# Kernel tuning notes

Measured on AMD Instinct MI355X. Metric: run time of the kernel, lower is better.

Reference implementation:

```python
import jax, jax.numpy as jnp
import numpy as np

D = 512
H = 8
HD = D // H
EPS = 1e-8


def setup_inputs() -> dict:
    key = jax.random.key(0)
    ks = jax.random.split(key, 16)
    B, S = 4, 2048
    s = lambda n: 1.0 / np.sqrt(n)
    inp = {
        "gene_emb": jax.random.normal(ks[0], (B, S, D), jnp.float32),
        "expr_emb": jax.random.normal(ks[1], (B, S, D), jnp.float32),
        "M": jax.random.uniform(ks[2], (B, S, S), jnp.float32),
        # weights stored (in, out) so y = x @ W + b
        "W_fused": jax.random.normal(ks[3], (2 * D, D), jnp.float32) * s(2 * D),
        "b_fused": jnp.zeros((D,), jnp.float32),
        "W_Q": jax.random.normal(ks[4], (D, D), jnp.float32) * s(D),
        "b_Q": jnp.zeros((D,), jnp.float32),
        "W_K": jax.random.normal(ks[5], (D, D), jnp.float32) * s(D),
        "b_K": jnp.zeros((D,), jnp.float32),
        "W_V": jax.random.normal(ks[6], (D, D), jnp.float32) * s(D),
        "b_V": jnp.zeros((D,), jnp.float32),
        "W_O": jax.random.normal(ks[7], (D, D), jnp.float32) * s(D),
        "b_O": jnp.zeros((D,), jnp.float32),
    }
    return inp


def reference(gene_emb, expr_emb, M, W_fused, b_fused, W_Q, b_Q, W_K, b_K, W_V, b_V, W_O, b_O):
    B, S, _ = gene_emb.shape
    scale = HD ** (-0.5)
    fused = jnp.concatenate([gene_emb, expr_emb], axis=-1) @ W_fused + b_fused
    # (B,S,D) -> (B,H,S,HD)
    split = lambda x: x.reshape(B, S, H, HD).transpose(0, 2, 1, 3)
    Q = split(fused @ W_Q + b_Q)
    K = split(fused @ W_K + b_K)
    V = split(expr_emb @ W_V + b_V)
    scores = jnp.einsum("bhqd,bhkd->bhqk", Q, K) * scale
    Mg = M[:, None, :, :]  # broadcast over heads
    scores = scores * Mg
    attn = jax.nn.softmax(scores, axis=-1)
    A_sparse = attn * Mg
    norm = jnp.sum(jnp.abs(A_sparse), axis=-1, keepdims=True) + EPS
    A_bar = A_sparse / norm
    out = jnp.einsum("bhqk,bhkd->bhqd", A_bar, V)
    out = out.transpose(0, 2, 1, 3).reshape(B, S, D)
    return out @ W_O + b_O
```

## Files before the change

kernel.cpp:

```cpp
#include <hip/hip_runtime.h>

typedef unsigned short u16;
typedef __attribute__((ext_vector_type(8))) short bf16x8_t;
typedef __attribute__((ext_vector_type(4))) float f32x4_t;
typedef __attribute__((ext_vector_type(16))) float f32x16_t;

__device__ __forceinline__ u16 f2bf(float x){
  union { float f; unsigned u; } v; v.f = x;
  unsigned r = v.u + 0x7FFFu + ((v.u >> 16) & 1u);
  return (u16)(r >> 16);
}
__device__ __forceinline__ float bf2f(u16 h){
  union { unsigned u; float f; } v; v.u = ((unsigned)h) << 16;
  return v.f;
}
__device__ __forceinline__ unsigned pack_hi16(float a, float b){
  union { float f; unsigned u; } x, y; x.f = a; y.f = b;
  return (x.u >> 16) | (y.u & 0xFFFF0000u);
}

__device__ __forceinline__ void gl2lds16(const u16* g, u16* l){
  __builtin_amdgcn_global_load_lds((const __attribute__((address_space(1))) void*)g,
                                   (__attribute__((address_space(3))) void*)l, 16, 0, 0);
}

__global__ __launch_bounds__(256) void split_concat_kernel(
    const float* __restrict__ gene, const float* __restrict__ expr,
    u16* __restrict__ Xh, u16* __restrict__ Xl)
{
  size_t e = ((size_t)blockIdx.x * 256 + threadIdx.x) * 4;
  int row = (int)(e >> 10);
  int col = (int)(e & 1023);
  const float* src = (col < 512) ? (gene + (size_t)row * 512 + col)
                                 : (expr + (size_t)row * 512 + (col - 512));
  float4 v = *(const float4*)src;
  float a[4] = {v.x, v.y, v.z, v.w};
  u16 hs[4], ls[4];
#pragma unroll
  for (int i = 0; i < 4; i++){
    hs[i] = f2bf(a[i]);
    ls[i] = f2bf(a[i] - bf2f(hs[i]));
  }
  *(uint2*)(Xh + e) = make_uint2(hs[0] | ((unsigned)hs[1] << 16), hs[2] | ((unsigned)hs[3] << 16));
  *(uint2*)(Xl + e) = make_uint2(ls[0] | ((unsigned)ls[1] << 16), ls[2] | ((unsigned)ls[3] << 16));
}

__global__ __launch_bounds__(256) void transpose_all_kernel(
    const float* __restrict__ Wf, const float* __restrict__ Wq,
    const float* __restrict__ Wk, const float* __restrict__ Wv,
    const float* __restrict__ Wo,
    u16* __restrict__ Wfth, u16* __restrict__ Wftl,
    u16* __restrict__ Wqth, u16* __restrict__ Wkth,
    u16* __restrict__ Wvth, u16* __restrict__ Woth)
{
  __shared__ float t[64][65];
  int id = blockIdx.x;
  const float* W; u16* Th; u16* Tl; int K, kx, ny;
  if (id < 128){ W = Wf; Th = Wfth; Tl = Wftl; K = 1024; kx = id >> 3; ny = id & 7; }
  else {
    int tt = id - 128; int wi = tt >> 6; tt &= 63; kx = tt >> 3; ny = tt & 7; K = 512;
    W  = (wi == 0) ? Wq  : (wi == 1) ? Wk  : (wi == 2) ? Wv  : Wo;
    Th = (wi == 0) ? Wqth: (wi == 1) ? Wkth: (wi == 2) ? Wvth: Woth;
    Tl = nullptr;
  }
  int k0 = kx * 64, n0 = ny * 64;
  int tid = threadIdx.x;
  int r = tid >> 4;
  int c4 = (tid & 15) * 4;
#pragma unroll
  for (int p = 0; p < 4; p++){
    int k = p * 16 + r;
    float4 v = *(const float4*)(W + (size_t)(k0 + k) * 512 + n0 + c4);
    t[c4 + 0][k] = v.x; t[c4 + 1][k] = v.y; t[c4 + 2][k] = v.z; t[c4 + 3][k] = v.w;
  }
  __syncthreads();
#pragma unroll
  for (int p = 0; p < 4; p++){
    int n = p * 16 + r;
    u16 hs[4], ls[4];
#pragma unroll
    for (int i = 0; i < 4; i++){
      float x = t[n][c4 + i];
      hs[i] = f2bf(x);
      ls[i] = f2bf(x - bf2f(hs[i]));
    }
    size_t o = (size_t)(n0 + n) * K + k0 + c4;
    *(uint2*)(Th + o) = make_uint2(hs[0] | ((unsigned)hs[1] << 16), hs[2] | ((unsigned)hs[3] << 16));
    if (Tl)
      *(uint2*)(Tl + o) = make_uint2(ls[0] | ((unsigned)ls[1] << 16), ls[2] | ((unsigned)ls[3] << 16));
  }
}

template<int SPLITS, int MODE, int DUAL>
__global__ __launch_bounds__(256, 2) void gemm_kernel(
    const u16* __restrict__ Ah, const u16* __restrict__ Al, int lda,
    const u16* __restrict__ Bh0, const u16* __restrict__ Bl0,
    const u16* __restrict__ Bh1, int K,
    const float* __restrict__ bias0, const float* __restrict__ bias1,
    void* __restrict__ out0, void* __restrict__ out1, void* __restrict__ outsec,
    float sc0, float sc1)
{
  __shared__ __align__(16) u16 sAh[128 * 32];
  __shared__ __align__(16) u16 sAl[SPLITS >= 2 ? 128 * 32 : 8];
  __shared__ __align__(16) u16 sBh[64 * 32];
  __shared__ __align__(16) u16 sBl[SPLITS == 3 ? 64 * 32 : 8];
  int tid = threadIdx.x;
  int lane = tid & 63, w = tid >> 6, quad = lane >> 4, l15 = lane & 15;
  int wm = w & 1, wn = w >> 1;
  int lid = (int)(blockIdx.y * gridDim.x + blockIdx.x);
  int side = DUAL ? (lid >> 9) : 0;
  int l = lid & 511;
  int m0 = (((l & 7) << 3) | ((l >> 3) & 7)) * 128;
  int n0 = (l >> 6) * 64;
  const u16* Bh = (DUAL && side) ? Bh1 : Bh0;
  const float* bias = (DUAL && side) ? bias1 : bias0;
  void* o0 = (DUAL && side) ? outsec : out0;
  float sc = (DUAL && side) ? sc1 : sc0;

  f32x4_t acc[4][2];
#pragma unroll
  for (int i = 0; i < 4; i++)
#pragma unroll
    for (int j = 0; j < 2; j++)
#pragma unroll
      for (int r = 0; r < 4; r++) acc[i][j][r] = 0.f;

  int lrow = lane >> 2;
  int swzS = ((lane >> 2) & 3) ^ ((lane >> 4) & 3);
  int gkq  = ((lane & 3) ^ swzS) * 8;
  const u16* pAh0 = Ah + (size_t)(m0 + w * 32 + lrow) * lda + gkq;
  const u16* pAh1 = Ah + (size_t)(m0 + w * 32 + 16 + lrow) * lda + gkq;
  const u16* pAl0 = (SPLITS >= 2) ? Al + (size_t)(m0 + w * 32 + lrow) * lda + gkq : nullptr;
  const u16* pAl1 = (SPLITS >= 2) ? Al + (size_t)(m0 + w * 32 + 16 + lrow) * lda + gkq : nullptr;
  const u16* pBh0 = Bh + (size_t)(n0 + w * 16 + lrow) * K + gkq;
  const u16* pBl0 = (SPLITS == 3) ? Bl0 + (size_t)(n0 + w * 16 + lrow) * K + gkq : nullptr;
  u16* dAh = sAh + w * 1024;
  u16* dAl = sAl + w * 1024;
  u16* dBh = sBh + w * 512;
  u16* dBl = sBl + w * 512;

  int pq = (quad ^ ((l15 & 3) ^ ((l15 >> 2) & 3))) * 8;

  for (int k0 = 0; k0 < K; k0 += 32){
    __syncthreads();
    gl2lds16(pAh0 + k0, dAh);
    gl2lds16(pAh1 + k0, dAh + 512);
    if constexpr (SPLITS >= 2){
      gl2lds16(pAl0 + k0, dAl);
      gl2lds16(pAl1 + k0, dAl + 512);
    }
    gl2lds16(pBh0 + k0, dBh);
    if constexpr (SPLITS == 3)
      gl2lds16(pBl0 + k0, dBl);
    __syncthreads();

    bf16x8_t aH[4], aL[4], bH[2], bL[2];
#pragma unroll
    for (int mi = 0; mi < 4; mi++){
      int ad = (wm * 64 + mi * 16 + l15) * 32 + pq;
      aH[mi] = *(const bf16x8_t*)&sAh[ad];
      if constexpr (SPLITS >= 2) aL[mi] = *(const bf16x8_t*)&sAl[ad];
    }
#pragma unroll
    for (int ni = 0; ni < 2; ni++){
      int bd = (wn * 32 + ni * 16 + l15) * 32 + pq;
      bH[ni] = *(const bf16x8_t*)&sBh[bd];
      if constexpr (SPLITS == 3) bL[ni] = *(const bf16x8_t*)&sBl[bd];
    }
#pragma unroll
    for (int mi = 0; mi < 4; mi++)
#pragma unroll
      for (int ni = 0; ni < 2; ni++){
        acc[mi][ni] = __builtin_amdgcn_mfma_f32_16x16x32_bf16(aH[mi], bH[ni], acc[mi][ni], 0, 0, 0);
        if constexpr (SPLITS == 3)
          acc[mi][ni] = __builtin_amdgcn_mfma_f32_16x16x32_bf16(aH[mi], bL[ni], acc[mi][ni], 0, 0, 0);
        if constexpr (SPLITS >= 2)
          acc[mi][ni] = __builtin_amdgcn_mfma_f32_16x16x32_bf16(aL[mi], bH[ni], acc[mi][ni], 0, 0, 0);
      }
  }

#pragma unroll
  for (int mi = 0; mi < 4; mi++)
#pragma unroll
    for (int ni = 0; ni < 2; ni++){
      int gn = n0 + wn * 32 + ni * 16 + l15;
      float bs = bias[gn];
      int gm0 = m0 + wm * 64 + mi * 16 + quad * 4;
#pragma unroll
      for (int r = 0; r < 4; r++){
        float v = acc[mi][ni][r] + bs;
        int gm = gm0 + r;
        if constexpr (MODE == 0){
          u16 hb = f2bf(v);
          ((u16*)o0)[(size_t)gm * 512 + gn] = hb;
          ((u16*)out1)[(size_t)gm * 512 + gn] = f2bf(v - bf2f(hb));
        } else if constexpr (MODE == 1){
          ((u16*)o0)[(size_t)gm * 512 + gn] = f2bf(v * sc);
        } else if constexpr (MODE == 2){
          int bb = gm >> 11, s = gm & 2047;
          int hh = gn >> 6, d = gn & 63;
          ((u16*)o0)[((size_t)((bb * 8 + hh) * 64 + d) << 11) + s] = f2bf(v);
        } else {
          ((float*)o0)[(size_t)gm * 512 + gn] = v;
        }
      }
    }
}

__global__ __launch_bounds__(256, 2) void flash_kernel(
    const u16* __restrict__ Qh, const u16* __restrict__ Kh,
    const u16* __restrict__ Vt, const float* __restrict__ Mm,
    u16* __restrict__ Oh)
{
  __shared__ __align__(16) u16 sAll[2][16384];
  int tid = threadIdx.x, lane = tid & 63, w = tid >> 6;
  int ql = lane & 31, hi = lane >> 5;
  int wq = w >> 1, wk = w & 1;
  int by = blockIdx.y, b = by >> 2, h0 = (by & 3) * 2;
  int q0 = blockIdx.x * 64;
  int q  = q0 + wq * 32 + ql;

  const u16* qp = Qh + ((size_t)(b * 2048 + q)) * 512 + h0 * 64 + hi * 8;
  bf16x8_t qf[2][4];
#pragma unroll
  for (int h = 0; h < 2; h++)
#pragma unroll
    for (int dt = 0; dt < 4; dt++)
      qf[h][dt] = *(const bf16x8_t*)(qp + h * 64 + dt * 16);

  int srow = lane >> 3, c8 = lane & 7;
  const u16* gK[4]; const u16* gV[4];
#pragma unroll
  for (int c = 0; c < 4; c++){
    int kv = wk * 32 + c * 8 + srow;
    int skey = ((c >> 1) << 2) | ((c & 1) << 1) | (srow & 1);
    gK[c] = Kh + ((size_t)(b * 2048 + kv)) * 512 + (h0 + wq) * 64 + ((c8 ^ skey) << 3);
    gV[c] = Vt + ((size_t)((b * 8 + h0 + wq) * 64 + kv)) * 2048 + ((c8 ^ srow) << 3);
  }
  int dO = wq * 4096 + wk * 2048;

  int phi = ((ql >> 3) & 1) * 16 + ((ql >> 2) & 1) * 8 + (ql >> 4) * 4 + (ql & 3);
  int kvL = wk * 32 + phi;
  int skr = ((ql >> 3) & 1) * 4 + ((ql >> 2) & 1) * 2 + (ql & 1);
  int kaddr[4];
#pragma unroll
  for (int dt = 0; dt < 4; dt++)
    kaddr[dt] = kvL * 64 + (((dt * 2 + hi) ^ skr) << 3);
  int vaddr[2][2];
#pragma unroll
  for (int dn = 0; dn < 2; dn++)
#pragma unroll
    for (int kt = 0; kt < 2; kt++)
      vaddr[dn][kt] = (dn * 32 + ql) * 64 + (((wk * 4 + kt * 2 + hi) ^ (ql & 7)) << 3);

  const float* mp = Mm + (size_t)b * (2048 * 2048) + (size_t)q * 2048 + wk * 32 + hi * 8;
  const int og[4] = {0, 16, 4, 20};

  float lp[2] = {0.f, 0.f};
  f32x16_t Oc[2][2];
#pragma unroll
  for (int h = 0; h < 2; h++)
#pragma unroll
    for (int dn = 0; dn < 2; dn++)
#pragma unroll
      for (int r = 0; r < 16; r++) Oc[h][dn][r] = 0.f;

#define STAGE(B, KK) do {                                              \
    _Pragma("unroll")                                                  \
    for (int c = 0; c < 4; c++){                                       \
      gl2lds16(gK[c] + (size_t)(KK) * 512, &sAll[B][dO + c * 512]);    \
      gl2lds16(gV[c] + (KK),               &sAll[B][8192 + dO + c * 512]); \
    }                                                                  \
  } while (0)

  STAGE(0, 0);
  f32x4_t Mc[4], Mn[4];
#pragma unroll
  for (int g = 0; g < 4; g++) Mc[g] = *(const f32x4_t*)(mp + og[g]);
  __syncthreads();

  for (int t = 0; t < 32; ++t){
    int ph = t & 1;
    bool nx = t < 31;
    if (nx) STAGE(ph ^ 1, (t + 1) * 64);
    if (nx){
#pragma unroll
      for (int g = 0; g < 4; g++) Mn[g] = *(const f32x4_t*)(mp + (t + 1) * 64 + og[g]);
    }
    const u16* kb = &sAll[ph][0];
    const u16* vb = &sAll[ph][8192];

#pragma unroll
    for (int h = 0; h < 2; ++h){
      const u16* kbh = kb + h * 4096;
      const u16* vbh = vb + h * 4096;

      f32x16_t S;
#pragma unroll
      for (int r = 0; r < 16; r++) S[r] = 0.f;
#pragma unroll
      for (int dt = 0; dt < 4; dt++){
        bf16x8_t kf = *(const bf16x8_t*)&kbh[kaddr[dt]];
        S = __builtin_amdgcn_mfma_f32_32x32x16_bf16(kf, qf[h][dt], S, 0, 0, 0);
      }

      float p[16];
#pragma unroll
      for (int g = 0; g < 4; g++)
#pragma unroll
        for (int e = 0; e < 4; e++){
          float m = Mc[g][e];
          float v = m * __builtin_amdgcn_exp2f(S[g * 4 + e] * m);
          lp[h] += v;
          p[g * 4 + e] = v;
        }
#pragma unroll
      for (int kt = 0; kt < 2; kt++){
        union { unsigned u[4]; bf16x8_t v8; } pb;
        pb.u[0] = pack_hi16(p[kt * 4 + 0], p[kt * 4 + 1]);
        pb.u[1] = pack_hi16(p[kt * 4 + 2], p[kt * 4 + 3]);
        pb.u[2] = pack_hi16(p[kt * 4 + 8], p[kt * 4 + 9]);
        pb.u[3] = pack_hi16(p[kt * 4 + 10], p[kt * 4 + 11]);
#pragma unroll
        for (int dn = 0; dn < 2; dn++){
          bf16x8_t vf = *(const bf16x8_t*)&vbh[vaddr[dn][kt]];
          Oc[h][dn] = __builtin_amdgcn_mfma_f32_32x32x16_bf16(vf, pb.v8, Oc[h][dn], 0, 0, 0);
        }
      }
    }

    __syncthreads();
    if (nx){
#pragma unroll
      for (int g = 0; g < 4; g++) Mc[g] = Mn[g];
    }
  }
#undef STAGE

  lp[0] += __shfl_xor(lp[0], 32);
  lp[1] += __shfl_xor(lp[1], 32);

  float* red = (float*)&sAll[0][0];
  float* lpr = red + 8192;
  if (wk){
#pragma unroll
    for (int h = 0; h < 2; h++){
#pragma unroll
      for (int dn = 0; dn < 2; dn++)
#pragma unroll
        for (int rq = 0; rq < 4; rq++){
          f32x4_t o;
          o[0] = Oc[h][dn][rq * 4 + 0]; o[1] = Oc[h][dn][rq * 4 + 1];
          o[2] = Oc[h][dn][rq * 4 + 2]; o[3] = Oc[h][dn][rq * 4 + 3];
          *(f32x4_t*)&red[((((wq * 2 + h) * 2 + dn) * 4 + rq) * 64 + lane) * 4] = o;
        }
      lpr[(wq * 2 + h) * 64 + lane] = lp[h];
    }
  }
  __syncthreads();
  if (!wk){
#pragma unroll
    for (int h = 0; h < 2; h++){
      float li = lp[h] + lpr[(wq * 2 + h) * 64 + lane];
      float inv = 1.0f / li;
      size_t ob = ((size_t)(b * 2048 + q)) * 512 + (h0 + h) * 64;
#pragma unroll
      for (int dn = 0; dn < 2; dn++)
#pragma unroll
        for (int rq = 0; rq < 4; rq++){
          f32x4_t o = *(const f32x4_t*)&red[((((wq * 2 + h) * 2 + dn) * 4 + rq) * 64 + lane) * 4];
          float v0 = (Oc[h][dn][rq * 4 + 0] + o[0]) * inv;
          float v1 = (Oc[h][dn][rq * 4 + 1] + o[1]) * inv;
          float v2 = (Oc[h][dn][rq * 4 + 2] + o[2]) * inv;
          float v3 = (Oc[h][dn][rq * 4 + 3] + o[3]) * inv;
          int d0 = dn * 32 + rq * 8 + hi * 4;
          unsigned w0 = (unsigned)f2bf(v0) | ((unsigned)f2bf(v1) << 16);
          unsigned w1 = (unsigned)f2bf(v2) | ((unsigned)f2bf(v3) << 16);
          *(uint2*)(Oh + ob + d0) = make_uint2(w0, w1);
        }
    }
  }
}

extern "C" void kernel_launch(void* const* d_in, const int* in_sizes, int n_in,
                              void* d_out, int out_size, void* d_ws, size_t ws_size,
                              hipStream_t stream)
{
  const float* gene = (const float*)d_in[0];
  const float* expr = (const float*)d_in[1];
  const float* Mm   = (const float*)d_in[2];
  const float* Wf   = (const float*)d_in[3];
  const float* bfv  = (const float*)d_in[4];
  const float* Wq   = (const float*)d_in[5];
  const float* bq   = (const float*)d_in[6];
  const float* Wk   = (const float*)d_in[7];
  const float* bk   = (const float*)d_in[8];
  const float* Wv   = (const float*)d_in[9];
  const float* bv   = (const float*)d_in[10];
  const float* Wo   = (const float*)d_in[11];
  const float* bo   = (const float*)d_in[12];
  float* out = (float*)d_out;

  char* ws = (char*)d_ws;
  size_t off = 0;
  auto alloc = [&](size_t bytes) -> void* {
    void* p = (void*)(ws + off);
    off += (bytes + 255) & ~(size_t)255;
    return p;
  };
  u16* Xh   = (u16*)alloc(8192ull * 1024 * 2);
  u16* Xl   = (u16*)alloc(8192ull * 1024 * 2);
  u16* Wfth = (u16*)alloc(512ull * 1024 * 2);
  u16* Wftl = (u16*)alloc(512ull * 1024 * 2);
  u16* Wqth = (u16*)alloc(512ull * 512 * 2);
  u16* Wkth = (u16*)alloc(512ull * 512 * 2);
  u16* Wvth = (u16*)alloc(512ull * 512 * 2);
  u16* Woth = (u16*)alloc(512ull * 512 * 2);
  u16* Fh   = (u16*)alloc(8192ull * 512 * 2);
  u16* Fl   = (u16*)alloc(8192ull * 512 * 2);
  u16* Qh   = (u16*)alloc(8192ull * 512 * 2);
  u16* Kh   = (u16*)alloc(8192ull * 512 * 2);
  u16* Vt   = (u16*)alloc(8192ull * 512 * 2);
  u16* Oh = Xh;

  const float QSC = 0.1803368801f;

  split_concat_kernel<<<8192, 256, 0, stream>>>(gene, expr, Xh, Xl);
  transpose_all_kernel<<<384, 256, 0, stream>>>(Wf, Wq, Wk, Wv, Wo,
                                                Wfth, Wftl, Wqth, Wkth, Wvth, Woth);

  gemm_kernel<3, 0, 0><<<dim3(64, 8), 256, 0, stream>>>(
      Xh, Xl, 1024, Wfth, Wftl, nullptr, 1024, bfv, nullptr, Fh, Fl, nullptr, 1.f, 1.f);
  gemm_kernel<2, 1, 1><<<dim3(64, 16), 256, 0, stream>>>(
      Fh, Fl, 512, Wqth, nullptr, Wkth, 512, bq, bk, Qh, nullptr, Kh, QSC, 1.f);
  gemm_kernel<2, 2, 0><<<dim3(64, 8), 256, 0, stream>>>(
      Xh + 512, Xl + 512, 1024, Wvth, nullptr, nullptr, 512, bv, nullptr, Vt, nullptr, nullptr, 1.f, 1.f);
  flash_kernel<<<dim3(32, 16), 256, 0, stream>>>(Qh, Kh, Vt, Mm, Oh);
  gemm_kernel<1, 3, 0><<<dim3(64, 8), 256, 0, stream>>>(
      Oh, nullptr, 512, Woth, nullptr, nullptr, 512, bo, nullptr, out, nullptr, nullptr, 1.f, 1.f);

  (void)in_sizes; (void)n_in; (void)out_size; (void)ws_size;
}
```

Before: 302.0 us.

## Double-buffer LDS tiles in GEMM to overlap global loads with MFMA

Result: no change. 301.4 us (-0.2%).

```diff
diff --git a/kernel.cpp b/kernel.cpp
--- a/kernel.cpp
+++ b/kernel.cpp
@@ -100,10 +100,10 @@
     void* __restrict__ out0, void* __restrict__ out1, void* __restrict__ outsec,
     float sc0, float sc1)
 {
-  __shared__ __align__(16) u16 sAh[128 * 32];
-  __shared__ __align__(16) u16 sAl[SPLITS >= 2 ? 128 * 32 : 8];
-  __shared__ __align__(16) u16 sBh[64 * 32];
-  __shared__ __align__(16) u16 sBl[SPLITS == 3 ? 64 * 32 : 8];
+  __shared__ __align__(16) u16 sAh[2][128 * 32];
+  __shared__ __align__(16) u16 sAl[SPLITS >= 2 ? 2 : 1][SPLITS >= 2 ? 128 * 32 : 8];
+  __shared__ __align__(16) u16 sBh[2][64 * 32];
+  __shared__ __align__(16) u16 sBl[SPLITS == 3 ? 2 : 1][SPLITS == 3 ? 64 * 32 : 8];
   int tid = threadIdx.x;
   int lane = tid & 63, w = tid >> 6, quad = lane >> 4, l15 = lane & 15;
   int wm = w & 1, wn = w >> 1;
@@ -134,38 +134,42 @@
   const u16* pAl1 = (SPLITS >= 2) ? Al + (size_t)(m0 + w * 32 + 16 + lrow) * lda + gkq : nullptr;
   const u16* pBh0 = Bh + (size_t)(n0 + w * 16 + lrow) * K + gkq;
   const u16* pBl0 = (SPLITS == 3) ? Bl0 + (size_t)(n0 + w * 16 + lrow) * K + gkq : nullptr;
-  u16* dAh = sAh + w * 1024;
-  u16* dAl = sAl + w * 1024;
-  u16* dBh = sBh + w * 512;
-  u16* dBl = sBl + w * 512;
 
   int pq = (quad ^ ((l15 & 3) ^ ((l15 >> 2) & 3))) * 8;
 
-  for (int k0 = 0; k0 < K; k0 += 32){
-    __syncthreads();
-    gl2lds16(pAh0 + k0, dAh);
-    gl2lds16(pAh1 + k0, dAh + 512);
-    if constexpr (SPLITS >= 2){
-      gl2lds16(pAl0 + k0, dAl);
-      gl2lds16(pAl1 + k0, dAl + 512);
-    }
-    gl2lds16(pBh0 + k0, dBh);
-    if constexpr (SPLITS == 3)
-      gl2lds16(pBl0 + k0, dBl);
-    __syncthreads();
+#define STAGEG(B, KK) do {                                                 \
+    gl2lds16(pAh0 + (KK), &sAh[B][w * 1024]);                              \
+    gl2lds16(pAh1 + (KK), &sAh[B][w * 1024 + 512]);                        \
+    if constexpr (SPLITS >= 2){                                            \
+      gl2lds16(pAl0 + (KK), &sAl[B][w * 1024]);                            \
+      gl2lds16(pAl1 + (KK), &sAl[B][w * 1024 + 512]);                      \
+    }                                                                      \
+    gl2lds16(pBh0 + (KK), &sBh[B][w * 512]);                               \
+    if constexpr (SPLITS == 3)                                             \
+      gl2lds16(pBl0 + (KK), &sBl[B][w * 512]);                             \
+  } while (0)
+
+  STAGEG(0, 0);
+  __syncthreads();
+
+  int T = K >> 5;
+  for (int t = 0; t < T; ++t){
+    int ph = t & 1;
+    bool nx = (t + 1) < T;
+    if (nx) STAGEG(ph ^ 1, (t + 1) * 32);
 
     bf16x8_t aH[4], aL[4], bH[2], bL[2];
 #pragma unroll
     for (int mi = 0; mi < 4; mi++){
       int ad = (wm * 64 + mi * 16 + l15) * 32 + pq;
-      aH[mi] = *(const bf16x8_t*)&sAh[ad];
-      if constexpr (SPLITS >= 2) aL[mi] = *(const bf16x8_t*)&sAl[ad];
+      aH[mi] = *(const bf16x8_t*)&sAh[ph][ad];
+      if constexpr (SPLITS >= 2) aL[mi] = *(const bf16x8_t*)&sAl[ph][ad];
     }
 #pragma unroll
     for (int ni = 0; ni < 2; ni++){
       int bd = (wn * 32 + ni * 16 + l15) * 32 + pq;
-      bH[ni] = *(const bf16x8_t*)&sBh[bd];
-      if constexpr (SPLITS == 3) bL[ni] = *(const bf16x8_t*)&sBl[bd];
+      bH[ni] = *(const bf16x8_t*)&sBh[ph][bd];
+      if constexpr (SPLITS == 3) bL[ni] = *(const bf16x8_t*)&sBl[ph][bd];
     }
 #pragma unroll
     for (int mi = 0; mi < 4; mi++)
@@ -177,7 +181,10 @@
         if constexpr (SPLITS >= 2)
           acc[mi][ni] = __builtin_amdgcn_mfma_f32_16x16x32_bf16(aL[mi], bH[ni], acc[mi][ni], 0, 0, 0);
       }
-  }
+
+    if (nx) __syncthreads();
+  }
+#undef STAGEG
 
 #pragma unroll
   for (int mi = 0; mi < 4; mi++)
```
